# Optimization experiments

Measured on AMD Instinct MI355X. Metric: run time of the kernel, lower is better.

The kernel has to match this reference:

```python
import jax, jax.numpy as jnp
import numpy as np

NUM_WORDS = 256  # max word index + 1 (sentinel row NUM_WORDS used to drop non-first-occurrence scatters)


def setup_inputs() -> dict:
    key = jax.random.key(0)
    ks = jax.random.split(key, 8)
    B, S, H, R, D, C = 16, 512, 768, 8, 512, 27
    hidden_states = jax.random.normal(ks[0], (B, S, H), jnp.float32)
    word_ids = jnp.sort(jax.random.randint(ks[1], (B, S), 0, NUM_WORDS), axis=-1)
    relations_positions = jax.random.randint(ks[2], (B, R), 0, S)
    w_rel = jax.random.normal(ks[3], (H,), jnp.float32) / np.sqrt(H).astype(np.float32)
    b_rel = jnp.zeros((1,), jnp.float32)
    w1 = jax.random.normal(ks[4], (2 * H, D), jnp.float32) / np.sqrt(2 * H).astype(np.float32)
    b1 = jnp.zeros((D,), jnp.float32)
    w2 = jax.random.normal(ks[5], (D, C), jnp.float32) / np.sqrt(D).astype(np.float32)
    b2 = jnp.zeros((C,), jnp.float32)
    return dict(hidden_states=hidden_states, word_ids=word_ids,
                relations_positions=relations_positions,
                w_rel=w_rel, b_rel=b_rel, w1=w1, b1=b1, w2=w2, b2=b2)


def reference(hidden_states, word_ids, relations_positions, w_rel, b_rel, w1, b1, w2, b2):
    B, S, H = hidden_states.shape
    # relational logits: Linear(H, 1).squeeze(-1)  -> [B, S]
    rel_logits = jnp.einsum('bsh,h->bs', hidden_states, w_rel) + b_rel

    # first_hidden_states[i, w] = hidden_states[i, j] at the FIRST token j of word w
    # (torch loop keys on word_id != prev_word_id; word_ids are monotone per row)
    first_occ = jnp.concatenate(
        [jnp.ones((B, 1), bool), word_ids[:, 1:] != word_ids[:, :-1]], axis=1)
    tgt = jnp.where(first_occ, word_ids, NUM_WORDS)  # route non-first tokens to sentinel row
    batch_idx = jnp.arange(B)[:, None]
    first_hidden = (jnp.zeros((B, NUM_WORDS + 1, H), hidden_states.dtype)
                    .at[batch_idx, tgt].set(hidden_states))[:, :NUM_WORDS]  # [B, W, H]

    # gather relation token embeddings -> [B, R, H]
    rel_hidden = jnp.take_along_axis(
        hidden_states, relations_positions[:, :, None], axis=1)

    # concat([word_embed, rel_embed]) @ w1 == word_embed @ w1[:H] + rel_embed @ w1[H:]
    h_word = jnp.einsum('bwh,hd->bwd', first_hidden, w1[:H])   # [B, W, D]
    h_rel = jnp.einsum('brh,hd->brd', rel_hidden, w1[H:])      # [B, R, D]
    hmid = jax.nn.relu(h_word[:, None, :, :] + h_rel[:, :, None, :] + b1)  # [B, R, W, D]
    role_logits = jnp.einsum('brwd,dc->brwc', hmid, w2) + b2   # [B, R, W, C]

    return rel_logits, role_logits
```

## Files before the change

kernel.cpp:

```cpp
#include <hip/hip_runtime.h>
#include <hip/hip_bf16.h>

#define BB 16
#define SS 512
#define HH 768
#define RR 8
#define DD 512
#define CC 27
#define WW 256

typedef __attribute__((ext_vector_type(8))) short short8;
typedef __attribute__((ext_vector_type(4))) float f32x4;

union PKu { unsigned short us[8]; uint4 u4; short8 s8; };

__device__ __forceinline__ unsigned short f32_to_bf16_rne(float v) {
    unsigned int u = __float_as_uint(v);
    unsigned int r = u + 0x7fffu + ((u >> 16) & 1u);
    return (unsigned short)(r >> 16);
}
__device__ __forceinline__ float bf16_to_f32(unsigned short u) {
    return __uint_as_float(((unsigned int)u) << 16);
}

__device__ __forceinline__ void glds16(const void* g, void* l) {
    __builtin_amdgcn_global_load_lds(
        (const __attribute__((address_space(1))) unsigned int*)g,
        (__attribute__((address_space(3))) unsigned int*)l, 16, 0, 0);
}


__global__ __launch_bounds__(512) void k_front(
    const float* __restrict__ hidden, const int* __restrict__ word_ids,
    const int* __restrict__ relpos, const float4* __restrict__ wrel4,
    const float* __restrict__ b_rel, const float* __restrict__ w1,
    const float* __restrict__ w2, float* __restrict__ out0,
    unsigned short* __restrict__ first_hidden,
    unsigned short* __restrict__ rel_hidden,
    unsigned short* __restrict__ w1t, unsigned short* __restrict__ w2t) {
    int bid = blockIdx.x, t = threadIdx.x;
    int wv = t >> 6, lane = t & 63;
    if (bid < 256) {
#pragma unroll
        for (int it = 0; it < 4; ++it) {
            int row = bid * 32 + it * 8 + wv;
            const float4* hid4 = (const float4*)hidden + (size_t)row * (HH / 4);
            float4 v[3];
            float acc = 0.f;
#pragma unroll
            for (int j = 0; j < 3; ++j) {
                v[j] = hid4[j * 64 + lane];
                float4 w = wrel4[j * 64 + lane];
                acc += v[j].x * w.x + v[j].y * w.y + v[j].z * w.z + v[j].w * w.w;
            }
#pragma unroll
            for (int off = 32; off > 0; off >>= 1) acc += __shfl_xor(acc, off, 64);
            if (lane == 0) out0[row] = acc + b_rel[0];
            int wid = word_ids[row];
            int s = row & (SS - 1);
            int prev = (s == 0) ? -1 : word_ids[row - 1];
            if (wid != prev) {
                int b = row >> 9;
                unsigned short* dst = first_hidden + (size_t)(b * WW + wid) * HH;
#pragma unroll
                for (int j = 0; j < 3; ++j) {
                    union { unsigned short us[4]; uint2 u2; } pk;
                    pk.us[0] = f32_to_bf16_rne(v[j].x);
                    pk.us[1] = f32_to_bf16_rne(v[j].y);
                    pk.us[2] = f32_to_bf16_rne(v[j].z);
                    pk.us[3] = f32_to_bf16_rne(v[j].w);
                    *(uint2*)(dst + j * 256 + lane * 4) = pk.u2;
                }
            }
        }
        return;
    }
    int x = bid - 256;
    if (x < 96) {
        __shared__ unsigned short tile[2][64][72];
        int half = t >> 8, tt = t & 255;
        int job = x * 2 + half;
        int kt = job >> 3, nt = job & 7;
        int i = tt >> 2, j4 = (tt & 3) * 16;
        const float* src = w1 + (size_t)(kt * 64 + i) * DD + nt * 64 + j4;
#pragma unroll
        for (int v = 0; v < 4; ++v) {
            float4 f = *(const float4*)(src + v * 4);
            tile[half][i][j4 + v * 4 + 0] = f32_to_bf16_rne(f.x);
            tile[half][i][j4 + v * 4 + 1] = f32_to_bf16_rne(f.y);
            tile[half][i][j4 + v * 4 + 2] = f32_to_bf16_rne(f.z);
            tile[half][i][j4 + v * 4 + 3] = f32_to_bf16_rne(f.w);
        }
        __syncthreads();
        int jj = tt >> 2, cb = (tt & 3) * 16;
        union { unsigned short us[16]; uint4 u4[2]; } ov;
#pragma unroll
        for (int v = 0; v < 16; ++v) ov.us[v] = tile[half][cb + v][jj];
        unsigned short* dst = w1t + (size_t)(nt * 64 + jj) * (2 * HH) + kt * 64 + cb;
        *(uint4*)(dst) = ov.u4[0];
        *(uint4*)(dst + 8) = ov.u4[1];
    } else if (x == 96) {
        for (int idx = t; idx < 32 * DD; idx += 512) {
            int n = idx >> 9, k = idx & (DD - 1);
            float v = (n < CC) ? w2[(size_t)k * CC + n] : 0.f;
            w2t[n * DD + k] = f32_to_bf16_rne(v);
        }
    } else {
        __shared__ int pres[WW];
        int b = x - 97;
        if (t < WW) pres[t] = 0;
        __syncthreads();
        pres[word_ids[b * SS + t]] = 1;
        __syncthreads();
        if (t < WW && !pres[t]) {
            uint4 z = {0u, 0u, 0u, 0u};
            unsigned short* dst = first_hidden + (size_t)(b * WW + t) * HH;
#pragma unroll 4
            for (int c = 0; c < 96; ++c) *(uint4*)(dst + c * 8) = z;
        }
        for (int idx = t; idx < RR * 96; idx += 512) {
            int rr = idx / 96, c = idx % 96;
            int pos = relpos[b * RR + rr];
            const float* srow = hidden + (size_t)(b * SS + pos) * HH + c * 8;
            PKu pk;
#pragma unroll
            for (int e = 0; e < 8; ++e) pk.us[e] = f32_to_bf16_rne(srow[e]);
            *(uint4*)(rel_hidden + (size_t)(b * RR + rr) * HH + c * 8) = pk.u4;
        }
    }
}

__global__ __launch_bounds__(256) void k_gemm(
    const unsigned short* __restrict__ first_hidden,
    const unsigned short* __restrict__ rel_hidden,
    const unsigned short* __restrict__ w1t, const float* __restrict__ b1,
    unsigned short* __restrict__ h_word, unsigned short* __restrict__ h_rel) {
    __shared__ __align__(16) unsigned char a_s[16384];
    __shared__ __align__(16) unsigned char b_s[16384];
    int bid = blockIdx.x;
    int nt, m0;
    bool isw;
    if (bid < 512) {
        int xcd = bid & 7, k = bid >> 3;
        int mt = xcd + 8 * (k & 7);
        nt = k >> 3;
        isw = true;
        m0 = mt * 64;
    } else {
        int jj = bid - 512;
        isw = false;
        m0 = (jj >> 3) * 64;
        nt = jj & 7;
    }
    const unsigned short* A = isw ? first_hidden : rel_hidden;
    unsigned short* C = isw ? h_word : h_rel;
    int kbase = isw ? 0 : HH;
    int t = threadIdx.x;
    int wv = t >> 6, lane = t & 63;
    int wr = wv >> 1, wc = wv & 1;
    int q = lane >> 4, r = lane & 15;

    const unsigned char* aP[2];
    const unsigned char* bP[2];
    unsigned lofa[2], lofb[2];
#pragma unroll
    for (int g = 0; g < 2; ++g) {
        int ci = g * 256 + t;
        int row = ci >> 3, ch = ci & 7;
        int sc = ch ^ (row & 7);
        aP[g] = (const unsigned char*)A + (size_t)(m0 + row) * (HH * 2) + sc * 16;
        lofa[g] = ci * 16;
        bP[g] = (const unsigned char*)w1t + (size_t)(nt * 64 + row) * (2 * HH * 2)
                + (size_t)kbase * 2 + sc * 16;
        lofb[g] = ci * 16;
    }
    int arow[2], brow[2];
#pragma unroll
    for (int mi = 0; mi < 2; ++mi) arow[mi] = wr * 32 + mi * 16 + r;
#pragma unroll
    for (int ni = 0; ni < 2; ++ni) brow[ni] = wc * 32 + ni * 16 + r;

    f32x4 acc[2][2];
#pragma unroll
    for (int mi = 0; mi < 2; ++mi)
#pragma unroll
        for (int ni = 0; ni < 2; ++ni) acc[mi][ni] = (f32x4){0.f, 0.f, 0.f, 0.f};

#pragma unroll
    for (int g = 0; g < 2; ++g) glds16(aP[g], a_s + lofa[g]);
#pragma unroll
    for (int g = 0; g < 2; ++g) glds16(bP[g], b_s + lofb[g]);
    __syncthreads();

    for (int kt = 0; kt < 12; ++kt) {
        if (kt < 11) {
            unsigned nb = ((kt + 1) & 1) * 8192;
#pragma unroll
            for (int g = 0; g < 2; ++g) glds16(aP[g] + (kt + 1) * 128, a_s + nb + lofa[g]);
#pragma unroll
            for (int g = 0; g < 2; ++g) glds16(bP[g] + (kt + 1) * 128, b_s + nb + lofb[g]);
        }
        unsigned bo = (kt & 1) * 8192;
#pragma unroll
        for (int ks = 0; ks < 2; ++ks) {
            int c = ks * 4 + q;
            short8 bfr[2];
#pragma unroll
            for (int ni = 0; ni < 2; ++ni)
                bfr[ni] = *(const short8*)(b_s + bo + brow[ni] * 128 +
                            ((c ^ (brow[ni] & 7)) << 4));
#pragma unroll
            for (int mi = 0; mi < 2; ++mi) {
                short8 af = *(const short8*)(a_s + bo + arow[mi] * 128 +
                            ((c ^ (arow[mi] & 7)) << 4));
                acc[mi][0] = __builtin_amdgcn_mfma_f32_16x16x32_bf16(
                    af, bfr[0], acc[mi][0], 0, 0, 0);
                acc[mi][1] = __builtin_amdgcn_mfma_f32_16x16x32_bf16(
                    af, bfr[1], acc[mi][1], 0, 0, 0);
            }
        }
        __syncthreads();
    }
    float bias[2];
#pragma unroll
    for (int ni = 0; ni < 2; ++ni) {
        int n = nt * 64 + wc * 32 + ni * 16 + r;
        bias[ni] = isw ? b1[n] : 0.f;
    }
#pragma unroll
    for (int mi = 0; mi < 2; ++mi) {
        int m = m0 + wr * 32 + mi * 16 + q * 4;
#pragma unroll
        for (int ni = 0; ni < 2; ++ni) {
            int n = nt * 64 + wc * 32 + ni * 16 + r;
#pragma unroll
            for (int reg = 0; reg < 4; ++reg)
                C[(size_t)(m + reg) * DD + n] =
                    f32_to_bf16_rne(acc[mi][ni][reg] + bias[ni]);
        }
    }
}

__global__ __launch_bounds__(512) void k_role(
    const unsigned short* __restrict__ h_word, const unsigned short* __restrict__ h_rel,
    const unsigned short* __restrict__ w2t, const float* __restrict__ b2,
    float* __restrict__ out_role) {
    int wt = blockIdx.x;
    int b  = blockIdx.y;
    int t  = threadIdx.x;
    __shared__ __align__(16) unsigned char hw_s[16384];
    __shared__ float hr_s[RR][DD];
    __shared__ __align__(16) unsigned char w2_s[32768];
    int wv = t >> 6, lane = t & 63;
#pragma unroll
    for (int i = 0; i < 2; ++i) {
        int row = wv * 2 + i;
        const unsigned short* src = h_word +
            (size_t)(b * WW + wt * 16 + row) * DD + ((lane ^ (row & 7)) * 8);
        glds16(src, hw_s + row * 1024 + lane * 16);
    }
#pragma unroll
    for (int i = 0; i < 4; ++i) {
        int row = wv * 4 + i;
        const unsigned short* src = w2t + row * DD + ((lane ^ (row & 7)) * 8);
        glds16(src, w2_s + row * 1024 + lane * 16);
    }
    {
        int rr = wv, c = lane;
        PKu hv;
        hv.u4 = *(const uint4*)(h_rel + (size_t)(b * RR + rr) * DD + c * 8);
        float4 o0, o1;
        o0.x = bf16_to_f32(hv.us[0]); o0.y = bf16_to_f32(hv.us[1]);
        o0.z = bf16_to_f32(hv.us[2]); o0.w = bf16_to_f32(hv.us[3]);
        o1.x = bf16_to_f32(hv.us[4]); o1.y = bf16_to_f32(hv.us[5]);
        o1.z = bf16_to_f32(hv.us[6]); o1.w = bf16_to_f32(hv.us[7]);
        *(float4*)&hr_s[rr][c * 8]     = o0;
        *(float4*)&hr_s[rr][c * 8 + 4] = o1;
    }
    __syncthreads();
    int q = lane >> 4, wl = lane & 15;
    int rr = wv;
    unsigned wlx = (wl & 7) << 4;
    f32x4 acc[2];
#pragma unroll
    for (int ni = 0; ni < 2; ++ni) acc[ni] = (f32x4){0.f, 0.f, 0.f, 0.f};

#pragma unroll 2
    for (int ks = 0; ks < DD / 32; ++ks) {
        int c = 4 * ks + q;
        short8 bfr[2];
#pragma unroll
        for (int ni = 0; ni < 2; ++ni) {
            int n = ni * 16 + wl;
            bfr[ni] = *(const short8*)(w2_s + n * 1024 + ((c ^ (n & 7)) << 4));
        }
        PKu hw;
        hw.u4 = *(const uint4*)(hw_s + wl * 1024 + ((unsigned)(c << 4) ^ wlx));
        const float* hrp = &hr_s[rr][ks * 32 + q * 8];
        float4 h0 = *(const float4*)(hrp);
        float4 h1 = *(const float4*)(hrp + 4);
        PKu pk;
        pk.us[0] = f32_to_bf16_rne(fmaxf(bf16_to_f32(hw.us[0]) + h0.x, 0.f));
        pk.us[1] = f32_to_bf16_rne(fmaxf(bf16_to_f32(hw.us[1]) + h0.y, 0.f));
        pk.us[2] = f32_to_bf16_rne(fmaxf(bf16_to_f32(hw.us[2]) + h0.z, 0.f));
        pk.us[3] = f32_to_bf16_rne(fmaxf(bf16_to_f32(hw.us[3]) + h0.w, 0.f));
        pk.us[4] = f32_to_bf16_rne(fmaxf(bf16_to_f32(hw.us[4]) + h1.x, 0.f));
        pk.us[5] = f32_to_bf16_rne(fmaxf(bf16_to_f32(hw.us[5]) + h1.y, 0.f));
        pk.us[6] = f32_to_bf16_rne(fmaxf(bf16_to_f32(hw.us[6]) + h1.z, 0.f));
        pk.us[7] = f32_to_bf16_rne(fmaxf(bf16_to_f32(hw.us[7]) + h1.w, 0.f));
#pragma unroll
        for (int ni = 0; ni < 2; ++ni)
            acc[ni] = __builtin_amdgcn_mfma_f32_16x16x32_bf16(
                pk.s8, bfr[ni], acc[ni], 0, 0, 0);
    }
#pragma unroll
    for (int ni = 0; ni < 2; ++ni) {
        int c = ni * 16 + wl;
        if (c < CC) {
#pragma unroll
            for (int reg = 0; reg < 4; ++reg) {
                int wg = wt * 16 + 4 * q + reg;
                out_role[(size_t)((b * RR + rr) * WW + wg) * CC + c] =
                    acc[ni][reg] + b2[c];
            }
        }
    }
}

extern "C" void kernel_launch(void* const* d_in, const int* in_sizes, int n_in,
                              void* d_out, int out_size, void* d_ws, size_t ws_size,
                              hipStream_t stream) {
    const float* hidden   = (const float*)d_in[0];
    const int*   word_ids = (const int*)d_in[1];
    const int*   relpos   = (const int*)d_in[2];
    const float* w_rel    = (const float*)d_in[3];
    const float* b_rel    = (const float*)d_in[4];
    const float* w1       = (const float*)d_in[5];
    const float* b1       = (const float*)d_in[6];
    const float* w2       = (const float*)d_in[7];
    const float* b2       = (const float*)d_in[8];

    float* out0 = (float*)d_out;
    float* out1 = out0 + BB * SS;

    unsigned short* first_hidden = (unsigned short*)d_ws;
    unsigned short* rel_hidden   = (unsigned short*)((char*)d_ws + 6291456);
    unsigned short* w1t          = (unsigned short*)((char*)d_ws + 6488064);
    unsigned short* w2t          = (unsigned short*)((char*)d_ws + 8060928);
    unsigned short* h_word       = (unsigned short*)((char*)d_ws + 8093696);
    unsigned short* h_rel        = (unsigned short*)((char*)d_ws + 12288000);

    k_front<<<369, 512, 0, stream>>>(
        hidden, word_ids, relpos, (const float4*)w_rel, b_rel, w1, w2,
        out0, first_hidden, rel_hidden, w1t, w2t);
    k_gemm<<<528, 256, 0, stream>>>(
        first_hidden, rel_hidden, w1t, b1, h_word, h_rel);
    k_role<<<dim3(WW / 16, BB), 512, 0, stream>>>(h_word, h_rel, w2t, b2, out1);
}
```

Measured before the change: 37.25 us.

## Fuse word GEMM with role head and compute relation GEMM in front kernel

Removes the separate GEMM kernel. The relation-token projection (h_rel) is now computed directly inside k_front, gathering the fp32 hidden rows and the bottom half of w1 on the fly. The word-embedding projection is fused with the ReLU and second GEMM into a new k_tail kernel that keeps h_word in shared memory. This drops one launch and the round-trip of h_word and rel_hidden through global memory. In exchange, k_tail runs only 128 blocks with about 150KB of LDS each, so occupancy is low and w1t is re-streamed by every block.

```diff
diff --git a/kernel.cpp b/kernel.cpp
--- a/kernel.cpp
+++ b/kernel.cpp
@@ -22,11 +22,22 @@
 __device__ __forceinline__ float bf16_to_f32(unsigned short u) {
     return __uint_as_float(((unsigned int)u) << 16);
 }
-
 __device__ __forceinline__ void glds16(const void* g, void* l) {
     __builtin_amdgcn_global_load_lds(
         (const __attribute__((address_space(1))) unsigned int*)g,
         (__attribute__((address_space(3))) unsigned int*)l, 16, 0, 0);
+}
+__device__ __forceinline__ uint4 pack8(float4 f0, float4 f1) {
+    PKu pk;
+    pk.us[0] = f32_to_bf16_rne(f0.x);
+    pk.us[1] = f32_to_bf16_rne(f0.y);
+    pk.us[2] = f32_to_bf16_rne(f0.z);
+    pk.us[3] = f32_to_bf16_rne(f0.w);
+    pk.us[4] = f32_to_bf16_rne(f1.x);
+    pk.us[5] = f32_to_bf16_rne(f1.y);
+    pk.us[6] = f32_to_bf16_rne(f1.z);
+    pk.us[7] = f32_to_bf16_rne(f1.w);
+    return pk.u4;
 }
 
 
@@ -36,8 +47,9 @@
     const float* __restrict__ b_rel, const float* __restrict__ w1,
     const float* __restrict__ w2, float* __restrict__ out0,
     unsigned short* __restrict__ first_hidden,
-    unsigned short* __restrict__ rel_hidden,
-    unsigned short* __restrict__ w1t, unsigned short* __restrict__ w2t) {
+    unsigned short* __restrict__ w1t, unsigned short* __restrict__ w2t,
+    unsigned short* __restrict__ h_rel) {
+    __shared__ __align__(16) unsigned char smem[25600];
     int bid = blockIdx.x, t = threadIdx.x;
     int wv = t >> 6, lane = t & 63;
     if (bid < 256) {
@@ -76,8 +88,8 @@
         return;
     }
     int x = bid - 256;
-    if (x < 96) {
-        __shared__ unsigned short tile[2][64][72];
+    if (x < 48) {
+        unsigned short (*tile)[64][72] = (unsigned short(*)[64][72])smem;
         int half = t >> 8, tt = t & 255;
         int job = x * 2 + half;
         int kt = job >> 3, nt = job & 7;
@@ -96,18 +108,18 @@
         union { unsigned short us[16]; uint4 u4[2]; } ov;
 #pragma unroll
         for (int v = 0; v < 16; ++v) ov.us[v] = tile[half][cb + v][jj];
-        unsigned short* dst = w1t + (size_t)(nt * 64 + jj) * (2 * HH) + kt * 64 + cb;
+        unsigned short* dst = w1t + (size_t)(nt * 64 + jj) * HH + kt * 64 + cb;
         *(uint4*)(dst) = ov.u4[0];
         *(uint4*)(dst + 8) = ov.u4[1];
-    } else if (x == 96) {
+    } else if (x == 48) {
         for (int idx = t; idx < 32 * DD; idx += 512) {
             int n = idx >> 9, k = idx & (DD - 1);
             float v = (n < CC) ? w2[(size_t)k * CC + n] : 0.f;
             w2t[n * DD + k] = f32_to_bf16_rne(v);
         }
-    } else {
-        __shared__ int pres[WW];
-        int b = x - 97;
+    } else if (x < 65) {
+        int* pres = (int*)smem;
+        int b = x - 49;
         if (t < WW) pres[t] = 0;
         __syncthreads();
         pres[word_ids[b * SS + t]] = 1;
@@ -118,210 +130,214 @@
 #pragma unroll 4
             for (int c = 0; c < 96; ++c) *(uint4*)(dst + c * 8) = z;
         }
-        for (int idx = t; idx < RR * 96; idx += 512) {
-            int rr = idx / 96, c = idx % 96;
-            int pos = relpos[b * RR + rr];
-            const float* srow = hidden + (size_t)(b * SS + pos) * HH + c * 8;
+    } else {
+        unsigned char* a_s = smem;
+        unsigned char* b_s = smem + 8192;
+        unsigned short (*tile)[72] = (unsigned short(*)[72])(smem + 16384);
+        int job = x - 65;
+        int mh = job >> 3, nt = job & 7;
+        int arow = t >> 3, as = t & 7;
+        int grow = mh * 64 + arow;
+        int bb = grow >> 3, rr = grow & 7;
+        int pos = relpos[bb * RR + rr];
+        const float* aSrc = hidden + (size_t)(bb * SS + pos) * HH
+                            + ((as ^ (arow & 7)) * 8);
+        unsigned a_dst = (unsigned)(arow * 128 + as * 16);
+        int bi = t >> 3, bc8 = (t & 7) * 8;
+        int tn = t >> 3, tsb = t & 7;
+        int tsrc = tsb ^ (tn & 7);
+        unsigned b_dst = (unsigned)(tn * 128 + tsb * 16);
+        int wm = wv >> 1, wnh = wv & 1;
+        int q = lane >> 4, r = lane & 15;
+        int amr = wm * 16 + r;
+        f32x4 acc[2];
+        acc[0] = (f32x4){0.f, 0.f, 0.f, 0.f};
+        acc[1] = (f32x4){0.f, 0.f, 0.f, 0.f};
+        for (int kt = 0; kt < 12; ++kt) {
+            {
+                float4 f0 = *(const float4*)(aSrc + kt * 64);
+                float4 f1 = *(const float4*)(aSrc + kt * 64 + 4);
+                *(uint4*)(a_s + a_dst) = pack8(f0, f1);
+                const float* bsrc = w1 + (size_t)(HH + kt * 64 + bi) * DD
+                                    + nt * 64 + bc8;
+                float4 g0 = *(const float4*)(bsrc);
+                float4 g1 = *(const float4*)(bsrc + 4);
+                *(uint4*)(&tile[bi][bc8]) = pack8(g0, g1);
+            }
+            __syncthreads();
+            {
+                PKu pk;
+#pragma unroll
+                for (int v = 0; v < 8; ++v) pk.us[v] = tile[tsrc * 8 + v][tn];
+                *(uint4*)(b_s + b_dst) = pk.u4;
+            }
+            __syncthreads();
+#pragma unroll
+            for (int ks = 0; ks < 2; ++ks) {
+                int c8 = ks * 4 + q;
+                short8 af = *(const short8*)(a_s + amr * 128 +
+                                             ((c8 ^ (amr & 7)) << 4));
+#pragma unroll
+                for (int ni = 0; ni < 2; ++ni) {
+                    int brow = wnh * 32 + ni * 16 + r;
+                    short8 bf = *(const short8*)(b_s + brow * 128 +
+                                                 ((c8 ^ (brow & 7)) << 4));
+                    acc[ni] = __builtin_amdgcn_mfma_f32_16x16x32_bf16(
+                        af, bf, acc[ni], 0, 0, 0);
+                }
+            }
+            __syncthreads();
+        }
+#pragma unroll
+        for (int ni = 0; ni < 2; ++ni) {
+            int col = nt * 64 + wnh * 32 + ni * 16 + r;
+#pragma unroll
+            for (int reg = 0; reg < 4; ++reg) {
+                int row = mh * 64 + wm * 16 + 4 * q + reg;
+                h_rel[(size_t)row * DD + col] = f32_to_bf16_rne(acc[ni][reg]);
+            }
+        }
+    }
+}
+
+__global__ __launch_bounds__(512) void k_tail(
+    const unsigned short* __restrict__ first_hidden,
+    const unsigned short* __restrict__ w1t,
+    const unsigned short* __restrict__ w2t,
+    const unsigned short* __restrict__ h_rel,
+    const float* __restrict__ b1, const float* __restrict__ b2,
+    float* __restrict__ out_role) {
+    __shared__ __align__(16) unsigned char a_s[49152];
+    __shared__ __align__(16) unsigned char b_s[32768];
+    __shared__ __align__(16) unsigned char hw_s[32768];
+    __shared__ __align__(16) unsigned char hr_s[8192];
+    __shared__ __align__(16) unsigned char w2_s[32768];
+    int j = blockIdx.x, t = threadIdx.x;
+    int wv = t >> 6, lane = t & 63, q = lane >> 4, r = lane & 15;
+    int b = j >> 3;
+    int R0 = j * 32;
+    int w0 = (j & 7) * 32;
+
+#pragma unroll
+    for (int g = 0; g < 6; ++g) {
+        int ci = g * 512 + t;
+        int row = ci / 96, s = ci % 96;
+        int sc = (s & ~7) | ((s & 7) ^ (row & 7));
+        glds16((const unsigned char*)first_hidden + (size_t)(R0 + row) * 1536 + sc * 16,
+               a_s + ci * 16);
+    }
+#pragma unroll
+    for (int g = 0; g < 4; ++g) {
+        int ci = g * 512 + t;
+        int n = ci >> 6, s = ci & 63;
+        int sc = (s & ~7) | ((s & 7) ^ (n & 7));
+        glds16((const unsigned char*)w2t + (size_t)n * 1024 + sc * 16, w2_s + ci * 16);
+    }
+    {
+        int rr = t >> 6, c = t & 63;
+        glds16((const unsigned char*)h_rel + (size_t)(b * RR + rr) * 1024 + c * 16,
+               hr_s + t * 16);
+    }
+    {
+        int bn = t >> 4, bs = t & 15;
+        int sc = (bs & ~7) | ((bs & 7) ^ (bn & 7));
+#pragma unroll
+        for (int g = 0; g < 2; ++g) {
+            int ci = g * 512 + t;
+            int n = ci >> 4, s = ci & 15;
+            int sc2 = (s & ~7) | ((s & 7) ^ (n & 7));
+            glds16((const unsigned char*)w1t + (size_t)n * 1536 + sc2 * 16,
+                   b_s + ci * 16);
+        }
+        (void)bn; (void)bs; (void)sc;
+    }
+    __syncthreads();
+
+    int wm = wv >> 2, wn = wv & 3;
+    int amr = wm * 16 + r;
+    int brow = wn * 16 + r;
+    for (int nt = 0; nt < 8; ++nt) {
+        f32x4 acc = (f32x4){0.f, 0.f, 0.f, 0.f};
+        for (int kt = 0; kt < 6; ++kt) {
+            int g = nt * 6 + kt;
+            if (g < 47) {
+                int nk = kt + 1, nn = nt;
+                if (nk == 6) { nk = 0; nn = nt + 1; }
+                unsigned dst = ((g + 1) & 1) * 16384;
+#pragma unroll
+                for (int g2 = 0; g2 < 2; ++g2) {
+                    int ci = g2 * 512 + t;
+                    int n = ci >> 4, s = ci & 15;
+                    int sc = (s & ~7) | ((s & 7) ^ (n & 7));
+                    glds16((const unsigned char*)w1t +
+                               (size_t)(nn * 64 + n) * 1536 + nk * 256 + sc * 16,
+                           b_s + dst + ci * 16);
+                }
+            }
+            unsigned bo = (g & 1) * 16384;
+#pragma unroll
+            for (int ks = 0; ks < 4; ++ks) {
+                int c8 = ks * 4 + q;
+                short8 af = *(const short8*)(a_s + amr * 1536 +
+                                ((kt * 16 + (c8 ^ (amr & 7))) << 4));
+                short8 bf = *(const short8*)(b_s + bo + brow * 256 +
+                                ((c8 ^ (brow & 7)) << 4));
+                acc = __builtin_amdgcn_mfma_f32_16x16x32_bf16(af, bf, acc, 0, 0, 0);
+            }
+            __syncthreads();
+        }
+        int col = nt * 64 + wn * 16 + r;
+        float b1v = b1[col];
+        int chs = col >> 3, cb2 = (col & 7) * 2;
+#pragma unroll
+        for (int reg = 0; reg < 4; ++reg) {
+            int row = wm * 16 + 4 * q + reg;
+            *(unsigned short*)(hw_s + row * 1024 + ((chs ^ (row & 7)) << 4) + cb2) =
+                f32_to_bf16_rne(acc[reg] + b1v);
+        }
+    }
+    __syncthreads();
+
+    int wl = lane & 15;
+    int rr = wv;
+#pragma unroll
+    for (int sub = 0; sub < 2; ++sub) {
+        f32x4 acc2[2];
+        acc2[0] = (f32x4){0.f, 0.f, 0.f, 0.f};
+        acc2[1] = (f32x4){0.f, 0.f, 0.f, 0.f};
+        int hrow = sub * 16 + wl;
+#pragma unroll 2
+        for (int ks = 0; ks < 16; ++ks) {
+            int c = 4 * ks + q;
+            short8 bfr[2];
+#pragma unroll
+            for (int ni = 0; ni < 2; ++ni) {
+                int n = ni * 16 + wl;
+                bfr[ni] = *(const short8*)(w2_s + n * 1024 + ((c ^ (n & 7)) << 4));
+            }
+            PKu hw, hr;
+            hw.u4 = *(const uint4*)(hw_s + hrow * 1024 + ((c ^ (hrow & 7)) << 4));
+            hr.u4 = *(const uint4*)(hr_s + rr * 1024 + c * 16);
             PKu pk;
 #pragma unroll
-            for (int e = 0; e < 8; ++e) pk.us[e] = f32_to_bf16_rne(srow[e]);
-            *(uint4*)(rel_hidden + (size_t)(b * RR + rr) * HH + c * 8) = pk.u4;
-        }
-    }
-}
-
-__global__ __launch_bounds__(256) void k_gemm(
-    const unsigned short* __restrict__ first_hidden,
-    const unsigned short* __restrict__ rel_hidden,
-    const unsigned short* __restrict__ w1t, const float* __restrict__ b1,
-    unsigned short* __restrict__ h_word, unsigned short* __restrict__ h_rel) {
-    __shared__ __align__(16) unsigned char a_s[16384];
-    __shared__ __align__(16) unsigned char b_s[16384];
-    int bid = blockIdx.x;
-    int nt, m0;
-    bool isw;
-    if (bid < 512) {
-        int xcd = bid & 7, k = bid >> 3;
-        int mt = xcd + 8 * (k & 7);
-        nt = k >> 3;
-        isw = true;
-        m0 = mt * 64;
-    } else {
-        int jj = bid - 512;
-        isw = false;
-        m0 = (jj >> 3) * 64;
-        nt = jj & 7;
-    }
-    const unsigned short* A = isw ? first_hidden : rel_hidden;
-    unsigned short* C = isw ? h_word : h_rel;
-    int kbase = isw ? 0 : HH;
-    int t = threadIdx.x;
-    int wv = t >> 6, lane = t & 63;
-    int wr = wv >> 1, wc = wv & 1;
-    int q = lane >> 4, r = lane & 15;
-
-    const unsigned char* aP[2];
-    const unsigned char* bP[2];
-    unsigned lofa[2], lofb[2];
-#pragma unroll
-    for (int g = 0; g < 2; ++g) {
-        int ci = g * 256 + t;
-        int row = ci >> 3, ch = ci & 7;
-        int sc = ch ^ (row & 7);
-        aP[g] = (const unsigned char*)A + (size_t)(m0 + row) * (HH * 2) + sc * 16;
-        lofa[g] = ci * 16;
-        bP[g] = (const unsigned char*)w1t + (size_t)(nt * 64 + row) * (2 * HH * 2)
-                + (size_t)kbase * 2 + sc * 16;
-        lofb[g] = ci * 16;
-    }
-    int arow[2], brow[2];
-#pragma unroll
-    for (int mi = 0; mi < 2; ++mi) arow[mi] = wr * 32 + mi * 16 + r;
-#pragma unroll
-    for (int ni = 0; ni < 2; ++ni) brow[ni] = wc * 32 + ni * 16 + r;
-
-    f32x4 acc[2][2];
-#pragma unroll
-    for (int mi = 0; mi < 2; ++mi)
-#pragma unroll
-        for (int ni = 0; ni < 2; ++ni) acc[mi][ni] = (f32x4){0.f, 0.f, 0.f, 0.f};
-
-#pragma unroll
-    for (int g = 0; g < 2; ++g) glds16(aP[g], a_s + lofa[g]);
-#pragma unroll
-    for (int g = 0; g < 2; ++g) glds16(bP[g], b_s + lofb[g]);
-    __syncthreads();
-
-    for (int kt = 0; kt < 12; ++kt) {
-        if (kt < 11) {
-            unsigned nb = ((kt + 1) & 1) * 8192;
-#pragma unroll
-            for (int g = 0; g < 2; ++g) glds16(aP[g] + (kt + 1) * 128, a_s + nb + lofa[g]);
-#pragma unroll
-            for (int g = 0; g < 2; ++g) glds16(bP[g] + (kt + 1) * 128, b_s + nb + lofb[g]);
-        }
-        unsigned bo = (kt & 1) * 8192;
-#pragma unroll
-        for (int ks = 0; ks < 2; ++ks) {
-            int c = ks * 4 + q;
-            short8 bfr[2];
+            for (int e = 0; e < 8; ++e)
+                pk.us[e] = f32_to_bf16_rne(
+                    fmaxf(bf16_to_f32(hw.us[e]) + bf16_to_f32(hr.us[e]), 0.f));
 #pragma unroll
             for (int ni = 0; ni < 2; ++ni)
-                bfr[ni] = *(const short8*)(b_s + bo + brow[ni] * 128 +
-                            ((c ^ (brow[ni] & 7)) << 4));
-#pragma unroll
-            for (int mi = 0; mi < 2; ++mi) {
-                short8 af = *(const short8*)(a_s + bo + arow[mi] * 128 +
-                            ((c ^ (arow[mi] & 7)) << 4));
-                acc[mi][0] = __builtin_amdgcn_mfma_f32_16x16x32_bf16(
-                    af, bfr[0], acc[mi][0], 0, 0, 0);
-                acc[mi][1] = __builtin_amdgcn_mfma_f32_16x16x32_bf16(
-                    af, bfr[1], acc[mi][1], 0, 0, 0);
-            }
-        }
-        __syncthreads();
-    }
-    float bias[2];
-#pragma unroll
-    for (int ni = 0; ni < 2; ++ni) {
-        int n = nt * 64 + wc * 32 + ni * 16 + r;
-        bias[ni] = isw ? b1[n] : 0.f;
-    }
-#pragma unroll
-    for (int mi = 0; mi < 2; ++mi) {
-        int m = m0 + wr * 32 + mi * 16 + q * 4;
+                acc2[ni] = __builtin_amdgcn_mfma_f32_16x16x32_bf16(
+                    pk.s8, bfr[ni], acc2[ni], 0, 0, 0);
+        }
 #pragma unroll
         for (int ni = 0; ni < 2; ++ni) {
-            int n = nt * 64 + wc * 32 + ni * 16 + r;
-#pragma unroll
-            for (int reg = 0; reg < 4; ++reg)
-                C[(size_t)(m + reg) * DD + n] =
-                    f32_to_bf16_rne(acc[mi][ni][reg] + bias[ni]);
-        }
-    }
-}
-
-__global__ __launch_bounds__(512) void k_role(
-    const unsigned short* __restrict__ h_word, const unsigned short* __restrict__ h_rel,
-    const unsigned short* __restrict__ w2t, const float* __restrict__ b2,
-    float* __restrict__ out_role) {
-    int wt = blockIdx.x;
-    int b  = blockIdx.y;
-    int t  = threadIdx.x;
-    __shared__ __align__(16) unsigned char hw_s[16384];
-    __shared__ float hr_s[RR][DD];
-    __shared__ __align__(16) unsigned char w2_s[32768];
-    int wv = t >> 6, lane = t & 63;
-#pragma unroll
-    for (int i = 0; i < 2; ++i) {
-        int row = wv * 2 + i;
-        const unsigned short* src = h_word +
-            (size_t)(b * WW + wt * 16 + row) * DD + ((lane ^ (row & 7)) * 8);
-        glds16(src, hw_s + row * 1024 + lane * 16);
-    }
-#pragma unroll
-    for (int i = 0; i < 4; ++i) {
-        int row = wv * 4 + i;
-        const unsigned short* src = w2t + row * DD + ((lane ^ (row & 7)) * 8);
-        glds16(src, w2_s + row * 1024 + lane * 16);
-    }
-    {
-        int rr = wv, c = lane;
-        PKu hv;
-        hv.u4 = *(const uint4*)(h_rel + (size_t)(b * RR + rr) * DD + c * 8);
-        float4 o0, o1;
-        o0.x = bf16_to_f32(hv.us[0]); o0.y = bf16_to_f32(hv.us[1]);
-        o0.z = bf16_to_f32(hv.us[2]); o0.w = bf16_to_f32(hv.us[3]);
-        o1.x = bf16_to_f32(hv.us[4]); o1.y = bf16_to_f32(hv.us[5]);
-        o1.z = bf16_to_f32(hv.us[6]); o1.w = bf16_to_f32(hv.us[7]);
-        *(float4*)&hr_s[rr][c * 8]     = o0;
-        *(float4*)&hr_s[rr][c * 8 + 4] = o1;
-    }
-    __syncthreads();
-    int q = lane >> 4, wl = lane & 15;
-    int rr = wv;
-    unsigned wlx = (wl & 7) << 4;
-    f32x4 acc[2];
-#pragma unroll
-    for (int ni = 0; ni < 2; ++ni) acc[ni] = (f32x4){0.f, 0.f, 0.f, 0.f};
-
-#pragma unroll 2
-    for (int ks = 0; ks < DD / 32; ++ks) {
-        int c = 4 * ks + q;
-        short8 bfr[2];
-#pragma unroll
-        for (int ni = 0; ni < 2; ++ni) {
-            int n = ni * 16 + wl;
-            bfr[ni] = *(const short8*)(w2_s + n * 1024 + ((c ^ (n & 7)) << 4));
-        }
-        PKu hw;
-        hw.u4 = *(const uint4*)(hw_s + wl * 1024 + ((unsigned)(c << 4) ^ wlx));
-        const float* hrp = &hr_s[rr][ks * 32 + q * 8];
-        float4 h0 = *(const float4*)(hrp);
-        float4 h1 = *(const float4*)(hrp + 4);
-        PKu pk;
-        pk.us[0] = f32_to_bf16_rne(fmaxf(bf16_to_f32(hw.us[0]) + h0.x, 0.f));
-        pk.us[1] = f32_to_bf16_rne(fmaxf(bf16_to_f32(hw.us[1]) + h0.y, 0.f));
-        pk.us[2] = f32_to_bf16_rne(fmaxf(bf16_to_f32(hw.us[2]) + h0.z, 0.f));
-        pk.us[3] = f32_to_bf16_rne(fmaxf(bf16_to_f32(hw.us[3]) + h0.w, 0.f));
-        pk.us[4] = f32_to_bf16_rne(fmaxf(bf16_to_f32(hw.us[4]) + h1.x, 0.f));
-        pk.us[5] = f32_to_bf16_rne(fmaxf(bf16_to_f32(hw.us[5]) + h1.y, 0.f));
-        pk.us[6] = f32_to_bf16_rne(fmaxf(bf16_to_f32(hw.us[6]) + h1.z, 0.f));
-        pk.us[7] = f32_to_bf16_rne(fmaxf(bf16_to_f32(hw.us[7]) + h1.w, 0.f));
-#pragma unroll
-        for (int ni = 0; ni < 2; ++ni)
-            acc[ni] = __builtin_amdgcn_mfma_f32_16x16x32_bf16(
-                pk.s8, bfr[ni], acc[ni], 0, 0, 0);
-    }
-#pragma unroll
-    for (int ni = 0; ni < 2; ++ni) {
-        int c = ni * 16 + wl;
-        if (c < CC) {
-#pragma unroll
-            for (int reg = 0; reg < 4; ++reg) {
-                int wg = wt * 16 + 4 * q + reg;
-                out_role[(size_t)((b * RR + rr) * WW + wg) * CC + c] =
-                    acc[ni][reg] + b2[c];
+            int c = ni * 16 + wl;
+            if (c < CC) {
+#pragma unroll
+                for (int reg = 0; reg < 4; ++reg) {
+                    int wg = w0 + sub * 16 + 4 * q + reg;
+                    out_role[(size_t)((b * RR + rr) * WW + wg) * CC + c] =
+                        acc2[ni][reg] + b2[c];
+                }
             }
         }
     }
@@ -344,16 +360,13 @@
     float* out1 = out0 + BB * SS;
 
     unsigned short* first_hidden = (unsigned short*)d_ws;
-    unsigned short* rel_hidden   = (unsigned short*)((char*)d_ws + 6291456);
-    unsigned short* w1t          = (unsigned short*)((char*)d_ws + 6488064);
-    unsigned short* w2t          = (unsigned short*)((char*)d_ws + 8060928);
-    unsigned short* h_word       = (unsigned short*)((char*)d_ws + 8093696);
-    unsigned short* h_rel        = (unsigned short*)((char*)d_ws + 12288000);
-
-    k_front<<<369, 512, 0, stream>>>(
+    unsigned short* w1t          = (unsigned short*)((char*)d_ws + 6291456);
+    unsigned short* w2t          = (unsigned short*)((char*)d_ws + 7077888);
+    unsigned short* h_rel        = (unsigned short*)((char*)d_ws + 7110656);
+
+    k_front<<<337, 512, 0, stream>>>(
         hidden, word_ids, relpos, (const float4*)w_rel, b_rel, w1, w2,
-        out0, first_hidden, rel_hidden, w1t, w2t);
-    k_gemm<<<528, 256, 0, stream>>>(
-        first_hidden, rel_hidden, w1t, b1, h_word, h_rel);
-    k_role<<<dim3(WW / 16, BB), 512, 0, stream>>>(h_word, h_rel, w2t, b2, out1);
-}
+        out0, first_hidden, w1t, w2t, h_rel);
+    k_tail<<<128, 512, 0, stream>>>(
+        first_hidden, w1t, w2t, h_rel, b1, b2, out1);
+}
```

After: 61.98 us. +66.4%, slower.
